# Performance work log

Hardware: AMD Instinct MI355X
Metric: run time of the kernel (lower is better)

## Reference

```python
import jax, jax.numpy as jnp
import numpy as np

ARITY = 2
DEPTH = 9          # max_depth: full tree has levels 0..DEPTH
H = 512            # hidden_size
V = 512            # vocab_size
B = 64             # batch
S = 64             # source length


def _preorder_perm(arity, depth):
    # map pre-order position -> flat level-order index
    offs = np.cumsum([0] + [arity ** d for d in range(depth + 1)])
    perm = []
    def rec(d, pos):
        perm.append(int(offs[d] + pos))
        if d < depth:
            for c in range(arity):
                rec(d + 1, pos * arity + c)
    rec(0, 0)
    return np.asarray(perm, dtype=np.int32)

PERM = jnp.asarray(_preorder_perm(ARITY, DEPTH))


def setup_inputs() -> dict:
    key = jax.random.key(0)
    ks = jax.random.split(key, 12)
    s = 0.05
    return {
        "root_hiddens": jax.random.normal(ks[0], (B, H), jnp.float32),
        "ann_emb": jax.random.normal(ks[1], (B, H), jnp.float32),
        "encoder_outputs": jax.random.normal(ks[2], (S, B, H), jnp.float32),
        "source_mask": jnp.ones((B, S), dtype=bool),
        # GRUCell params per child: input_size = 2H (attention concat)
        "w_ih": jax.random.normal(ks[3], (ARITY, 3 * H, 2 * H), jnp.float32) * s,
        "w_hh": jax.random.normal(ks[4], (ARITY, 3 * H, H), jnp.float32) * s,
        "b_ih": jax.random.normal(ks[5], (ARITY, 3 * H), jnp.float32) * s,
        "b_hh": jax.random.normal(ks[6], (ARITY, 3 * H), jnp.float32) * s,
        # hidden2vocab: Linear(H,2H) -> Sigmoid -> Linear(2H,V)
        "W1": jax.random.normal(ks[7], (2 * H, H), jnp.float32) * s,
        "b1": jax.random.normal(ks[8], (2 * H,), jnp.float32) * s,
        "W2": jax.random.normal(ks[9], (V, 2 * H), jnp.float32) * s,
        "b2": jax.random.normal(ks[10], (V,), jnp.float32) * s,
    }


def _gru(x, h, wih, whh, bih, bhh):
    # x: [B,n,2H], h: [B,n,H]; PyTorch GRUCell semantics
    gi = jnp.einsum('bni,gi->bng', x, wih) + bih
    gh = jnp.einsum('bnh,gh->bng', h, whh) + bhh
    i_r, i_z, i_n = jnp.split(gi, 3, axis=-1)
    h_r, h_z, h_n = jnp.split(gh, 3, axis=-1)
    r = jax.nn.sigmoid(i_r + h_r)
    z = jax.nn.sigmoid(i_z + h_z)
    n = jnp.tanh(i_n + r * h_n)
    return (1.0 - z) * n + z * h


def _forward(root_hiddens, ann_emb, encoder_outputs, source_mask,
             w_ih, w_hh, b_ih, b_hh, W1, b1, W2, b2):
    b = root_hiddens.shape[0]
    enc = encoder_outputs.transpose(1, 0, 2)        # [B,S,H]
    h = root_hiddens[:, None, :]                    # [B,1,H]
    prods = []
    for d in range(DEPTH + 1):
        # hidden2vocab at every node of this level
        hid = jax.nn.sigmoid(jnp.einsum('bnh,kh->bnk', h, W1) + b1)
        prods.append(jnp.einsum('bnk,vk->bnv', hid, W2) + b2)
        if d < DEPTH:
            # dot-product attention per node over source positions
            scores = jnp.einsum('bnh,bsh->bns', h, enc)
            scores = jnp.where(source_mask[:, None, :], scores, -1e9)
            a = jax.nn.softmax(scores, axis=-1)
            weighted = jnp.einsum('bns,bsh->bnh', a, enc)
            n = h.shape[1]
            x = jnp.concatenate(
                [jnp.broadcast_to(ann_emb[:, None, :], (b, n, H)), weighted],
                axis=-1)                             # [B,n,2H]
            children = [_gru(x, h, w_ih[c], w_hh[c], b_ih[c], b_hh[c])
                        for c in range(ARITY)]
            h = jnp.stack(children, axis=2).reshape(b, n * ARITY, H)
    out = jnp.concatenate(prods, axis=1)            # [B,N,V] level-order
    out = out[:, PERM, :]                           # pre-order, as torch yields
    return out.transpose(1, 0, 2)                   # [N,B,V] like pad_sequence


def reference(root_hiddens, ann_emb, encoder_outputs, source_mask,
              w_ih, w_hh, b_ih, b_hh, W1, b1, W2, b2):
    return _forward(root_hiddens, ann_emb, encoder_outputs, source_mask,
                    w_ih, w_hh, b_ih, b_hh, W1, b1, W2, b2)
```

## Files before the change

### kernel.cpp

```cpp
#include <hip/hip_runtime.h>


#define BATCH 64
#define HDIM  512

typedef float  floatx4 __attribute__((ext_vector_type(4)));
typedef float  f32x16  __attribute__((ext_vector_type(16)));
typedef short  short8  __attribute__((ext_vector_type(8)));

__device__ __forceinline__ float bf2f(unsigned short u) {
  union { unsigned int i; float f; } v; v.i = ((unsigned int)u) << 16; return v.f;
}
__device__ __forceinline__ unsigned short f2bf(float f) {
  union { float f; unsigned int i; } v; v.f = f;
  unsigned int x = v.i;
  return (unsigned short)((x + 0x7fffu + ((x >> 16) & 1u)) >> 16);
}
__device__ __forceinline__ float sigm(float x) { return 1.f / (1.f + __expf(-x)); }

__device__ __forceinline__ int preorder_idx(int d, int node) {
  int p = 0;
  for (int i = 1; i <= d; ++i) {
    int bit = (node >> (d - i)) & 1;
    p += 1 + bit * ((1 << (10 - i)) - 1);
  }
  return p;
}

__device__ __forceinline__ void gload_lds16(const void* g, void* l) {
  __builtin_amdgcn_global_load_lds(
      (const __attribute__((address_space(1))) unsigned int*)g,
      (__attribute__((address_space(3))) unsigned int*)l, 16, 0, 0);
}

__device__ __forceinline__ void stage_f32(unsigned short* ldst, const float* src) {
  float4 v0 = *(const float4*)src;
  float4 v1 = *(const float4*)(src + 4);
  union { unsigned short s[8]; float4 v; } u;
  u.s[0]=f2bf(v0.x); u.s[1]=f2bf(v0.y); u.s[2]=f2bf(v0.z); u.s[3]=f2bf(v0.w);
  u.s[4]=f2bf(v1.x); u.s[5]=f2bf(v1.y); u.s[6]=f2bf(v1.z); u.s[7]=f2bf(v1.w);
  *(float4*)ldst = u.v;
}

__device__ __forceinline__ void stage_split(unsigned short* dh, unsigned short* dl,
                                            const float* src) {
  float4 v0 = *(const float4*)src;
  float4 v1 = *(const float4*)(src + 4);
  float v[8] = {v0.x, v0.y, v0.z, v0.w, v1.x, v1.y, v1.z, v1.w};
  union { unsigned short s[8]; float4 q; } H, L;
  #pragma unroll
  for (int i = 0; i < 8; ++i) {
    unsigned short hb = f2bf(v[i]);
    H.s[i] = hb;
    L.s[i] = f2bf(v[i] - bf2f(hb));
  }
  *(float4*)dh = H.q;
  *(float4*)dl = L.q;
}

__global__ __launch_bounds__(256) void k_root(const float* __restrict__ root,
                                              float* __restrict__ h0,
                                              unsigned short* __restrict__ bh,
                                              unsigned short* __restrict__ bl) {
  int i = blockIdx.x * 256 + threadIdx.x;
  float v = root[i];
  h0[i] = v;
  int row = i >> 9, k = i & 511;
  int mt = row >> 5, r = row & 31, ktg = k >> 4, oct = (k >> 3) & 1, e = k & 7;
  size_t fo = ((size_t)(mt * 32 + ktg) * 64 + oct * 32 + r) * 8 + e;
  unsigned short hb = f2bf(v);
  bh[fo] = hb;
  bl[fo] = f2bf(v - bf2f(hb));
}

__global__ __launch_bounds__(256) void k_prep_wih(const float* __restrict__ wih,
                                                  unsigned short* __restrict__ dh,
                                                  unsigned short* __restrict__ dl) {
  int idx = blockIdx.x * 256 + threadIdx.x;
  int jr  = idx & 31;
  int oct = (idx >> 5) & 1;
  int ktg = (idx >> 6) & 31;
  int jt  = (idx >> 11) & 15;
  int cg  = idx >> 15;
  int c = cg / 3, g = cg % 3;
  int j = jt * 32 + jr, k = ktg * 16 + oct * 8;
  const float* src = wih + ((size_t)c * 1536 + g * 512 + j) * 1024 + 512 + k;
  float v[8];
  *(float4*)&v[0] = *(const float4*)src;
  *(float4*)&v[4] = *(const float4*)(src + 4);
  union { unsigned short s[8]; float4 q; } H, L;
  #pragma unroll
  for (int i = 0; i < 8; ++i) {
    unsigned short hb = f2bf(v[i]); H.s[i] = hb; L.s[i] = f2bf(v[i] - bf2f(hb));
  }
  *(float4*)(dh + (size_t)idx * 8) = H.q;
  *(float4*)(dl + (size_t)idx * 8) = L.q;
}

__global__ __launch_bounds__(256) void k_prep_whh(const float* __restrict__ whh,
                                                  unsigned short* __restrict__ dh,
                                                  unsigned short* __restrict__ dl) {
  int idx = blockIdx.x * 256 + threadIdx.x;
  int jr  = idx & 31;
  int oct = (idx >> 5) & 1;
  int ktg = (idx >> 6) & 31;
  int jt  = (idx >> 11) & 15;
  int cg  = idx >> 15;
  int c = cg / 3, g = cg % 3;
  int j = jt * 32 + jr, k = ktg * 16 + oct * 8;
  const float* src = whh + ((size_t)c * 1536 + g * 512 + j) * 512 + k;
  float v[8];
  *(float4*)&v[0] = *(const float4*)src;
  *(float4*)&v[4] = *(const float4*)(src + 4);
  union { unsigned short s[8]; float4 q; } H, L;
  #pragma unroll
  for (int i = 0; i < 8; ++i) {
    unsigned short hb = f2bf(v[i]); H.s[i] = hb; L.s[i] = f2bf(v[i] - bf2f(hb));
  }
  *(float4*)(dh + (size_t)idx * 8) = H.q;
  *(float4*)(dl + (size_t)idx * 8) = L.q;
}

__global__ __launch_bounds__(256) void k_prep_bf(const float* __restrict__ src,
                                                 unsigned short* __restrict__ db) {
  size_t i = ((size_t)blockIdx.x * 256 + threadIdx.x) * 8;
  stage_f32(db + i, src + i);
}

__global__ __launch_bounds__(256) void k_giann(const float* __restrict__ ann,
                                               const float* __restrict__ wih,
                                               float* __restrict__ giann) {
  __shared__ __align__(16) unsigned short lah[64*40], lal[64*40];
  __shared__ __align__(16) unsigned short lwh[64*40], lwl[64*40];
  int t = threadIdx.x, lane = t & 63, wv = t >> 6;
  int jbase = blockIdx.y * 64, c = blockIdx.z;
  const float* wih_c = wih + (size_t)c * 1536 * 1024;
  floatx4 acc[4];
  #pragma unroll
  for (int i = 0; i < 4; ++i) acc[i] = (floatx4)(0.f);
  int srow = t >> 2, skk = (t & 3) * 8;
  for (int k0 = 0; k0 < 512; k0 += 32) {
    stage_split(lah + srow*40 + skk, lal + srow*40 + skk,
                ann + (size_t)srow * 512 + k0 + skk);
    stage_split(lwh + srow*40 + skk, lwl + srow*40 + skk,
                wih_c + (size_t)(jbase + srow) * 1024 + k0 + skk);
    __syncthreads();
    int arow = wv * 16 + (lane & 15), kq = (lane >> 4) * 8;
    short8 ah = *(const short8*)(lah + arow*40 + kq);
    short8 al = *(const short8*)(lal + arow*40 + kq);
    #pragma unroll
    for (int nt = 0; nt < 4; ++nt) {
      int wo = (nt * 16 + (lane & 15)) * 40 + kq;
      short8 wh = *(const short8*)(lwh + wo);
      short8 wl = *(const short8*)(lwl + wo);
      acc[nt] = __builtin_amdgcn_mfma_f32_16x16x32_bf16(ah, wh, acc[nt], 0, 0, 0);
      acc[nt] = __builtin_amdgcn_mfma_f32_16x16x32_bf16(ah, wl, acc[nt], 0, 0, 0);
      acc[nt] = __builtin_amdgcn_mfma_f32_16x16x32_bf16(al, wh, acc[nt], 0, 0, 0);
    }
    __syncthreads();
  }
  int quad = lane >> 4, cl = lane & 15;
  #pragma unroll
  for (int nt = 0; nt < 4; ++nt) {
    int g = jbase + nt * 16 + cl;
    #pragma unroll
    for (int r = 0; r < 4; ++r) {
      int b = wv * 16 + quad * 4 + r;
      giann[((size_t)c * 64 + b) * 1536 + g] = acc[nt][r];
    }
  }
}

__global__ __launch_bounds__(256) void k_attn(const float* __restrict__ h,
                                              const float* __restrict__ enc,
                                              unsigned short* __restrict__ wgh,
                                              unsigned short* __restrict__ wgl,
                                              int d) {
  int lane = threadIdx.x & 63, wv = threadIdx.x >> 6;
  int m = blockIdx.x * 4 + wv;
  int b = m >> d;
  __shared__ __align__(16) float sh[4][512];
  {
    const float4* src = (const float4*)(h + (size_t)m * HDIM);
    float4* dst = (float4*)sh[wv];
    dst[lane] = src[lane];
    dst[lane + 64] = src[lane + 64];
  }
  __syncthreads();
  const float* hr = sh[wv];
  const float* er = enc + ((size_t)lane * BATCH + b) * HDIM;
  float sc = 0.f;
  for (int k = 0; k < HDIM; k += 8) {
    float4 w0 = *(const float4*)(er + k);
    float4 w1 = *(const float4*)(er + k + 4);
    sc += hr[k+0]*w0.x + hr[k+1]*w0.y + hr[k+2]*w0.z + hr[k+3]*w0.w;
    sc += hr[k+4]*w1.x + hr[k+5]*w1.y + hr[k+6]*w1.z + hr[k+7]*w1.w;
  }
  float mx = sc;
  #pragma unroll
  for (int off = 32; off; off >>= 1) mx = fmaxf(mx, __shfl_xor(mx, off));
  float e = __expf(sc - mx);
  float sum = e;
  #pragma unroll
  for (int off = 32; off; off >>= 1) sum += __shfl_xor(sum, off);
  float a = e / sum;
  float acc[8];
  #pragma unroll
  for (int i = 0; i < 8; ++i) acc[i] = 0.f;
  for (int s = 0; s < 64; ++s) {
    float as = __shfl(a, s);
    const float* ep = enc + ((size_t)s * BATCH + b) * HDIM + lane * 8;
    float4 w0 = *(const float4*)ep;
    float4 w1 = *(const float4*)(ep + 4);
    acc[0] += as * w0.x; acc[1] += as * w0.y; acc[2] += as * w0.z; acc[3] += as * w0.w;
    acc[4] += as * w1.x; acc[5] += as * w1.y; acc[6] += as * w1.z; acc[7] += as * w1.w;
  }
  union { unsigned short s[8]; float4 q; } H, L;
  #pragma unroll
  for (int i = 0; i < 8; ++i) {
    unsigned short hb = f2bf(acc[i]); H.s[i] = hb; L.s[i] = f2bf(acc[i] - bf2f(hb));
  }
  int mt = m >> 5, rr = m & 31;
  size_t fo = ((size_t)(mt * 32 + (lane >> 1)) * 64 + (lane & 1) * 32 + rr) * 8;
  *(float4*)(wgh + fo) = H.q;
  *(float4*)(wgl + fo) = L.q;
}

__global__ __launch_bounds__(256) void k_hid(const float* __restrict__ h,
                                             const unsigned short* __restrict__ W1b,
                                             const float* __restrict__ b1,
                                             unsigned short* __restrict__ hid) {
  __shared__ __align__(16) unsigned short la[64 * 40];
  __shared__ __align__(16) unsigned short lw[64 * 40];
  int t = threadIdx.x, lane = t & 63, wv = t >> 6;
  int mbase = blockIdx.x * 64, jbase = blockIdx.y * 64;
  floatx4 acc[4];
  #pragma unroll
  for (int i = 0; i < 4; ++i) acc[i] = (floatx4)(0.f);
  int srow = t >> 2, skk = (t & 3) * 8;
  for (int k0 = 0; k0 < 512; k0 += 32) {
    stage_f32(la + srow * 40 + skk, h + (size_t)(mbase + srow) * 512 + k0 + skk);
    *(float4*)(lw + srow * 40 + skk) =
        *(const float4*)(W1b + (size_t)(jbase + srow) * 512 + k0 + skk);
    __syncthreads();
    int arow = wv * 16 + (lane & 15);
    int kq = (lane >> 4) * 8;
    short8 af = *(const short8*)(la + arow * 40 + kq);
    #pragma unroll
    for (int nt = 0; nt < 4; ++nt) {
      short8 wf = *(const short8*)(lw + (nt * 16 + (lane & 15)) * 40 + kq);
      acc[nt] = __builtin_amdgcn_mfma_f32_16x16x32_bf16(af, wf, acc[nt], 0, 0, 0);
    }
    __syncthreads();
  }
  int quad = lane >> 4, cl = lane & 15;
  #pragma unroll
  for (int nt = 0; nt < 4; ++nt) {
    int j = jbase + nt * 16 + cl;
    float bias = b1[j];
    #pragma unroll
    for (int r = 0; r < 4; ++r) {
      int m = mbase + wv * 16 + quad * 4 + r;
      hid[(size_t)m * 1024 + j] = f2bf(sigm(acc[nt][r] + bias));
    }
  }
}

__global__ __launch_bounds__(256) void k_out(const unsigned short* __restrict__ hid,
                                             const unsigned short* __restrict__ W2b,
                                             const float* __restrict__ b2,
                                             float* __restrict__ out, int d) {
  __shared__ __align__(16) unsigned short la[64 * 40];
  __shared__ __align__(16) unsigned short lw[64 * 40];
  int t = threadIdx.x, lane = t & 63, wv = t >> 6;
  int mbase = blockIdx.x * 64, jbase = blockIdx.y * 64;
  floatx4 acc[4];
  #pragma unroll
  for (int i = 0; i < 4; ++i) acc[i] = (floatx4)(0.f);
  int srow = t >> 2, skk = (t & 3) * 8;
  for (int k0 = 0; k0 < 1024; k0 += 32) {
    *(float4*)(la + srow * 40 + skk) =
        *(const float4*)(hid + (size_t)(mbase + srow) * 1024 + k0 + skk);
    *(float4*)(lw + srow * 40 + skk) =
        *(const float4*)(W2b + (size_t)(jbase + srow) * 1024 + k0 + skk);
    __syncthreads();
    int arow = wv * 16 + (lane & 15);
    int kq = (lane >> 4) * 8;
    short8 af = *(const short8*)(la + arow * 40 + kq);
    #pragma unroll
    for (int nt = 0; nt < 4; ++nt) {
      short8 wf = *(const short8*)(lw + (nt * 16 + (lane & 15)) * 40 + kq);
      acc[nt] = __builtin_amdgcn_mfma_f32_16x16x32_bf16(af, wf, acc[nt], 0, 0, 0);
    }
    __syncthreads();
  }
  int quad = lane >> 4, cl = lane & 15;
  int nmask = (1 << d) - 1;
  int pv[4], bv[4];
  #pragma unroll
  for (int r = 0; r < 4; ++r) {
    int m = mbase + wv * 16 + quad * 4 + r;
    bv[r] = m >> d;
    pv[r] = preorder_idx(d, m & nmask);
  }
  #pragma unroll
  for (int nt = 0; nt < 4; ++nt) {
    int j = jbase + nt * 16 + cl;
    float bias = b2[j];
    #pragma unroll
    for (int r = 0; r < 4; ++r) {
      out[((size_t)pv[r] * BATCH + bv[r]) * 512 + j] = acc[nt][r] + bias;
    }
  }
}

#define MF32(a, b, c) __builtin_amdgcn_mfma_f32_32x32x16_bf16(a, b, c, 0, 0, 0)

__global__ __launch_bounds__(256, 2) void k_gru(const float* __restrict__ h,
                                             const unsigned short* __restrict__ wgh,
                                             const unsigned short* __restrict__ wgl,
                                             const unsigned short* __restrict__ hbh,
                                             const unsigned short* __restrict__ hbl,
                                             const unsigned short* __restrict__ wihh,
                                             const unsigned short* __restrict__ wihl,
                                             const unsigned short* __restrict__ whhh,
                                             const unsigned short* __restrict__ whhl,
                                             const float* __restrict__ bih,
                                             const float* __restrict__ bhh,
                                             const float* __restrict__ giann,
                                             float* __restrict__ hnext,
                                             unsigned short* __restrict__ nbh,
                                             unsigned short* __restrict__ nbl,
                                             int d, int M, int emit_bf) {
  __shared__ __align__(16) unsigned short smem[3][20 * 512];
  int t = threadIdx.x, lane = t & 63, wv = t >> 6;
  int wm = wv >> 1, wj = wv & 1;
  int c = blockIdx.z;
  int mbase = blockIdx.x * 128, jbase = blockIdx.y * 64;
  int jt0 = jbase >> 5;
  int mb32 = mbase >> 5;
  int mtcap = (M >> 5) - 1;

  f32x16 a_r[2], a_z[2], a_n[2], a_h[2];
  #pragma unroll
  for (int i = 0; i < 2; ++i) {
    a_r[i] = (f32x16)(0.f); a_z[i] = (f32x16)(0.f);
    a_n[i] = (f32x16)(0.f); a_h[i] = (f32x16)(0.f);
  }

  auto stage = [&](int it2, int buf2) {
    int pht = it2 >> 5, kt = it2 & 31;
    const unsigned short* Ah = pht ? hbh : wgh;
    const unsigned short* Al = pht ? hbl : wgl;
    const unsigned short* Wh = pht ? whhh : wihh;
    const unsigned short* Wl = pht ? whhl : wihl;
    #pragma unroll
    for (int q = 0; q < 5; ++q) {
      int f = wv * 5 + q;
      const unsigned short* src;
      if (f < 8) {
        int mtl = f >> 1;
        int mt = mb32 + mtl; if (mt > mtcap) mt = mtcap;
        const unsigned short* blob = (f & 1) ? Al : Ah;
        src = blob + ((size_t)(mt * 32 + kt) * 64 + lane) * 8;
      } else {
        int u = f - 8;
        int g = u >> 2, jtl = (u >> 1) & 1;
        const unsigned short* blob = (u & 1) ? Wl : Wh;
        src = blob + ((size_t)(((c * 3 + g) * 16 + jt0 + jtl) * 32 + kt) * 64
                      + lane) * 8;
      }
      gload_lds16(src, &smem[buf2][f * 512]);
    }
  };

  stage(0, 0);
  stage(1, 1);
  stage(2, 2);
  asm volatile("s_waitcnt vmcnt(10)" ::: "memory");
  __builtin_amdgcn_s_barrier();
  __builtin_amdgcn_sched_barrier(0);

  int buf = 0;
  #pragma unroll
  for (int ph = 0; ph < 2; ++ph) {
    f32x16* axr = ph ? a_h : a_n;
    for (int i2 = 0; i2 < 32; ++i2) {
      int it = ph * 32 + i2;
      const unsigned short* bb = smem[buf];
      short8 ah[2], al[2];
      #pragma unroll
      for (int mt = 0; mt < 2; ++mt) {
        int s = (wm * 2 + mt) * 2;
        ah[mt] = *(const short8*)(bb + s * 512 + lane * 8);
        al[mt] = *(const short8*)(bb + (s + 1) * 512 + lane * 8);
      }
      short8 w[3][2];
      #pragma unroll
      for (int g = 0; g < 3; ++g) {
        int s = 8 + (g * 2 + wj) * 2;
        w[g][0] = *(const short8*)(bb + s * 512 + lane * 8);
        w[g][1] = *(const short8*)(bb + (s + 1) * 512 + lane * 8);
      }
      asm volatile("s_waitcnt lgkmcnt(0)" ::: "memory");
      __builtin_amdgcn_sched_barrier(0);
      __builtin_amdgcn_s_barrier();
      __builtin_amdgcn_sched_barrier(0);
      if (it + 3 < 64) stage(it + 3, buf);
      __builtin_amdgcn_s_setprio(1);
      #pragma unroll
      for (int mt = 0; mt < 2; ++mt) {
        short8 AH = ah[mt], AL = al[mt];
        a_r[mt] = MF32(AH, w[0][0], a_r[mt]);
        a_r[mt] = MF32(AH, w[0][1], a_r[mt]);
        a_r[mt] = MF32(AL, w[0][0], a_r[mt]);
        a_z[mt] = MF32(AH, w[1][0], a_z[mt]);
        a_z[mt] = MF32(AH, w[1][1], a_z[mt]);
        a_z[mt] = MF32(AL, w[1][0], a_z[mt]);
        axr[mt] = MF32(AH, w[2][0], axr[mt]);
        axr[mt] = MF32(AH, w[2][1], axr[mt]);
        axr[mt] = MF32(AL, w[2][0], axr[mt]);
      }
      __builtin_amdgcn_s_setprio(0);
      __builtin_amdgcn_sched_barrier(0);
      if (it < 61) {
        asm volatile("s_waitcnt vmcnt(10)" ::: "memory");
      } else if (it == 61) {
        asm volatile("s_waitcnt vmcnt(5)" ::: "memory");
      } else {
        asm volatile("s_waitcnt vmcnt(0)" ::: "memory");
      }
      __builtin_amdgcn_sched_barrier(0);
      __builtin_amdgcn_s_barrier();
      __builtin_amdgcn_sched_barrier(0);
      buf = (buf == 2) ? 0 : buf + 1;
    }
  }

  unsigned short (*trh)[72] = (unsigned short(*)[72])(&smem[0][0]);
  unsigned short (*trl)[72] = (unsigned short(*)[72])(&smem[0][0] + 128 * 72);
  int cl = lane & 31;
  int j = jbase + wj * 32 + cl;
  float br  = bih[c * 1536 + j]        + bhh[c * 1536 + j];
  float bz  = bih[c * 1536 + 512 + j]  + bhh[c * 1536 + 512 + j];
  float bin = bih[c * 1536 + 1024 + j];
  float bhn = bhh[c * 1536 + 1024 + j];
  int rowoff = 4 * (lane >> 5);
  #pragma unroll
  for (int mt = 0; mt < 2; ++mt) {
    int mb0 = mbase + wm * 64 + mt * 32 + rowoff;
    #pragma unroll
    for (int r = 0; r < 16; ++r) {
      int m = mb0 + (r & 3) + 8 * (r >> 2);
      if (m < M) {
        int b = m >> d;
        const float* gp = giann + ((size_t)c * 64 + b) * 1536 + j;
        float rg = sigm(a_r[mt][r] + gp[0] + br);
        float zg = sigm(a_z[mt][r] + gp[512] + bz);
        float ng = tanhf(a_n[mt][r] + gp[1024] + bin + rg * (a_h[mt][r] + bhn));
        float hv = h[(size_t)m * 512 + j];
        float nh = (1.f - zg) * ng + zg * hv;
        hnext[(size_t)(2 * m + c) * 512 + j] = nh;
        if (emit_bf) {
          unsigned short hb = f2bf(nh);
          trh[m - mbase][j - jbase] = hb;
          trl[m - mbase][j - jbase] = f2bf(nh - bf2f(hb));
        }
      }
    }
  }
  if (emit_bf) {
    __syncthreads();
    int a = t >> 7;
    int row = t & 127;
    if (mbase + row < M) {
      const unsigned short* trp = a ? &trl[row][0] : &trh[row][0];
      unsigned short* dst = a ? nbl : nbh;
      int mp = 2 * (mbase + row) + c;
      int mtp = mp >> 5, rp = mp & 31;
      #pragma unroll
      for (int q = 0; q < 8; ++q) {
        int k = jbase + q * 8;
        int ktg = k >> 4, oct = (k >> 3) & 1;
        float4 v = *(const float4*)(trp + q * 8);
        *(float4*)(dst + ((size_t)(mtp * 32 + ktg) * 64 + oct * 32 + rp) * 8) = v;
      }
    }
  }
}

extern "C" void kernel_launch(void* const* d_in, const int* in_sizes, int n_in,
                              void* d_out, int out_size, void* d_ws, size_t ws_size,
                              hipStream_t stream) {
  const float* root = (const float*)d_in[0];
  const float* ann  = (const float*)d_in[1];
  const float* enc  = (const float*)d_in[2];
  const float* wih  = (const float*)d_in[4];
  const float* whh  = (const float*)d_in[5];
  const float* bih  = (const float*)d_in[6];
  const float* bhh  = (const float*)d_in[7];
  const float* W1   = (const float*)d_in[8];
  const float* b1   = (const float*)d_in[9];
  const float* W2   = (const float*)d_in[10];
  const float* b2   = (const float*)d_in[11];
  float* out = (float*)d_out;

  char* ws = (char*)d_ws;
  float* hA = (float*)ws;
  float* hB = (float*)(ws + (size_t)67108864);
  unsigned short* hid  = (unsigned short*)(ws + (size_t)100663296);
  unsigned short* wgh  = (unsigned short*)(ws + (size_t)134217728);
  unsigned short* wgl  = (unsigned short*)(ws + (size_t)150994944);
  unsigned short* hbEh = (unsigned short*)(ws + (size_t)167772160);
  unsigned short* hbEl = (unsigned short*)(ws + (size_t)184549376);
  unsigned short* hbOh = (unsigned short*)(ws + (size_t)201326592);
  unsigned short* hbOl = (unsigned short*)(ws + (size_t)209715200);
  float* giann         = (float*)(ws + (size_t)218103808);
  unsigned short* wihh = (unsigned short*)(ws + (size_t)218890240);
  unsigned short* wihl = (unsigned short*)(ws + (size_t)222035968);
  unsigned short* whhh = (unsigned short*)(ws + (size_t)225181696);
  unsigned short* whhl = (unsigned short*)(ws + (size_t)228327424);
  unsigned short* W1b  = (unsigned short*)(ws + (size_t)231473152);
  unsigned short* W2b  = (unsigned short*)(ws + (size_t)232521728);

  k_root<<<dim3(128), dim3(256), 0, stream>>>(root, hB, hbEh, hbEl);
  k_prep_wih<<<dim3(768), dim3(256), 0, stream>>>(wih, wihh, wihl);
  k_prep_whh<<<dim3(768), dim3(256), 0, stream>>>(whh, whhh, whhl);
  k_prep_bf<<<dim3(256), dim3(256), 0, stream>>>(W1, W1b);
  k_prep_bf<<<dim3(256), dim3(256), 0, stream>>>(W2, W2b);
  k_giann<<<dim3(1, 24, 2), dim3(256), 0, stream>>>(ann, wih, giann);

  float* hcur = hB;
  float* hnxt = hA;
  unsigned short *bhc = hbEh, *blc = hbEl, *bhn = hbOh, *bln = hbOl;
  for (int d = 0; d <= 9; ++d) {
    int n = 1 << d;
    int M = 64 * n;
    k_hid<<<dim3(M / 64, 16), dim3(256), 0, stream>>>(hcur, W1b, b1, hid);
    k_out<<<dim3(M / 64, 8), dim3(256), 0, stream>>>(hid, W2b, b2, out, d);
    if (d < 9) {
      k_attn<<<dim3(M / 4), dim3(256), 0, stream>>>(hcur, enc, wgh, wgl, d);
      k_gru<<<dim3((M + 127) / 128, 8, 2), dim3(256), 0, stream>>>(
          hcur, wgh, wgl, bhc, blc, wihh, wihl, whhh, whhl, bih, bhh, giann,
          hnxt, bhn, bln, d, M, d < 8 ? 1 : 0);
      float* tmp = hcur; hcur = hnxt; hnxt = tmp;
      unsigned short* ts;
      ts = bhc; bhc = bhn; bhn = ts;
      ts = blc; blc = bln; bln = ts;
    }
  }
}
```

Before: 2.334 ms.

## Use split-bf16 MFMA attention for deep levels and widen hid/out GEMM tiles

Adds a matrix-core attention kernel for tree depths 6 and up. Scores and the weighted sum are computed with split-bf16 (hi/lo) 32x32 MFMAs against encoder copies that are pre-transposed once per call, replacing the scalar per-node attention loop. It also widens the k_hid and k_out tiles to 256 output columns per block so each staged activation tile is reused four times. The new attention path only runs if the workspace is large enough, needs extra prep kernels and workspace, and the wider GEMM tiles produce fewer blocks at shallow levels.

Measured after the change: 1.999 ms. 14.3% less time.

```diff
diff --git a/kernel.cpp b/kernel.cpp
--- a/kernel.cpp
+++ b/kernel.cpp
@@ -121,6 +121,52 @@
   *(float4*)(dl + (size_t)idx * 8) = L.q;
 }
 
+__global__ __launch_bounds__(256) void k_prep_encB(const float* __restrict__ enc,
+                                                   unsigned short* __restrict__ dh,
+                                                   unsigned short* __restrict__ dl) {
+  int idx = blockIdx.x * 256 + threadIdx.x;
+  int jr  = idx & 31;
+  int oct = (idx >> 5) & 1;
+  int ktg = (idx >> 6) & 31;
+  int jt  = (idx >> 11) & 1;
+  int b   = idx >> 12;
+  int s = jt * 32 + jr, k = ktg * 16 + oct * 8;
+  const float* src = enc + ((size_t)s * 64 + b) * 512 + k;
+  float v[8];
+  *(float4*)&v[0] = *(const float4*)src;
+  *(float4*)&v[4] = *(const float4*)(src + 4);
+  union { unsigned short s_[8]; float4 q; } H, L;
+  #pragma unroll
+  for (int i = 0; i < 8; ++i) {
+    unsigned short hb = f2bf(v[i]); H.s_[i] = hb; L.s_[i] = f2bf(v[i] - bf2f(hb));
+  }
+  *(float4*)(dh + (size_t)idx * 8) = H.q;
+  *(float4*)(dl + (size_t)idx * 8) = L.q;
+}
+
+__global__ __launch_bounds__(256) void k_prep_encT(const float* __restrict__ enc,
+                                                   unsigned short* __restrict__ dh,
+                                                   unsigned short* __restrict__ dl) {
+  int idx = blockIdx.x * 256 + threadIdx.x;
+  int jr  = idx & 31;
+  int oct = (idx >> 5) & 1;
+  int ktg = (idx >> 6) & 3;
+  int jt  = (idx >> 8) & 15;
+  int b   = idx >> 12;
+  int hcol = jt * 32 + jr, s0 = ktg * 16 + oct * 8;
+  float v[8];
+  #pragma unroll
+  for (int e = 0; e < 8; ++e)
+    v[e] = enc[((size_t)(s0 + e) * 64 + b) * 512 + hcol];
+  union { unsigned short s_[8]; float4 q; } H, L;
+  #pragma unroll
+  for (int i = 0; i < 8; ++i) {
+    unsigned short hb = f2bf(v[i]); H.s_[i] = hb; L.s_[i] = f2bf(v[i] - bf2f(hb));
+  }
+  *(float4*)(dh + (size_t)idx * 8) = H.q;
+  *(float4*)(dl + (size_t)idx * 8) = L.q;
+}
+
 __global__ __launch_bounds__(256) void k_prep_bf(const float* __restrict__ src,
                                                  unsigned short* __restrict__ db) {
   size_t i = ((size_t)blockIdx.x * 256 + threadIdx.x) * 8;
@@ -226,44 +272,185 @@
   *(float4*)(wgl + fo) = L.q;
 }
 
+#define MF32(a, b, c) __builtin_amdgcn_mfma_f32_32x32x16_bf16(a, b, c, 0, 0, 0)
+
+__global__ __launch_bounds__(256, 1) void k_attn_mfma(
+    const unsigned short* __restrict__ hbh, const unsigned short* __restrict__ hbl,
+    const unsigned short* __restrict__ encBh, const unsigned short* __restrict__ encBl,
+    const unsigned short* __restrict__ encTh, const unsigned short* __restrict__ encTl,
+    unsigned short* __restrict__ wgh, unsigned short* __restrict__ wgl, int d) {
+  __shared__ __align__(16) float Sf[4608];
+  __shared__ __align__(16) unsigned short PAh[4096], PAl[4096];
+  int t = threadIdx.x, lane = t & 63, wv = t >> 6;
+  int mbase = blockIdx.x * 64;
+  int b = mbase >> d;
+  int mtg0 = mbase >> 5;
+  {
+    int mt = wv >> 1, sh2 = wv & 1;
+    f32x16 acc = (f32x16)(0.f);
+    size_t ab = ((size_t)(mtg0 + mt) * 32) * 512;
+    size_t bb = ((size_t)(b * 2 + sh2) * 32) * 512;
+    #pragma unroll 4
+    for (int kt = 0; kt < 32; ++kt) {
+      size_t o = ((size_t)kt * 64 + lane) * 8;
+      short8 ah = *(const short8*)(hbh + ab + o);
+      short8 al = *(const short8*)(hbl + ab + o);
+      short8 bh = *(const short8*)(encBh + bb + o);
+      short8 bl = *(const short8*)(encBl + bb + o);
+      acc = MF32(ah, bh, acc);
+      acc = MF32(ah, bl, acc);
+      acc = MF32(al, bh, acc);
+    }
+    int col = sh2 * 32 + (lane & 31);
+    int rb = mt * 32 + 4 * (lane >> 5);
+    #pragma unroll
+    for (int r = 0; r < 16; ++r)
+      Sf[(rb + (r & 3) + 8 * (r >> 2)) * 68 + col] = acc[r];
+  }
+  __syncthreads();
+  {
+    int row = t >> 2, q = t & 3;
+    float v[16];
+    const float* Sr = Sf + row * 68 + q * 16;
+    *(float4*)&v[0]  = *(const float4*)(Sr);
+    *(float4*)&v[4]  = *(const float4*)(Sr + 4);
+    *(float4*)&v[8]  = *(const float4*)(Sr + 8);
+    *(float4*)&v[12] = *(const float4*)(Sr + 12);
+    float mx = v[0];
+    #pragma unroll
+    for (int i = 1; i < 16; ++i) mx = fmaxf(mx, v[i]);
+    mx = fmaxf(mx, __shfl_xor(mx, 1));
+    mx = fmaxf(mx, __shfl_xor(mx, 2));
+    float sum = 0.f;
+    #pragma unroll
+    for (int i = 0; i < 16; ++i) { v[i] = __expf(v[i] - mx); sum += v[i]; }
+    sum += __shfl_xor(sum, 1);
+    sum += __shfl_xor(sum, 2);
+    float inv = 1.f / sum;
+    int wbase = ((row >> 5) * 4 + q) * 64;
+    #pragma unroll
+    for (int oct = 0; oct < 2; ++oct) {
+      union { unsigned short s_[8]; float4 q4; } H, L;
+      #pragma unroll
+      for (int e = 0; e < 8; ++e) {
+        float a = v[oct * 8 + e] * inv;
+        unsigned short hb = f2bf(a);
+        H.s_[e] = hb; L.s_[e] = f2bf(a - bf2f(hb));
+      }
+      int w = (wbase + oct * 32 + (row & 31)) * 8;
+      *(float4*)(PAh + w) = H.q4;
+      *(float4*)(PAl + w) = L.q4;
+    }
+  }
+  __syncthreads();
+  f32x16 o2[2][4];
+  #pragma unroll
+  for (int mt = 0; mt < 2; ++mt)
+    #pragma unroll
+    for (int jl = 0; jl < 4; ++jl) o2[mt][jl] = (f32x16)(0.f);
+  #pragma unroll
+  for (int ktg = 0; ktg < 4; ++ktg) {
+    short8 pah[2], pal[2];
+    #pragma unroll
+    for (int mt = 0; mt < 2; ++mt) {
+      pah[mt] = *(const short8*)(PAh + ((mt * 4 + ktg) * 64 + lane) * 8);
+      pal[mt] = *(const short8*)(PAl + ((mt * 4 + ktg) * 64 + lane) * 8);
+    }
+    #pragma unroll
+    for (int jl = 0; jl < 4; ++jl) {
+      int jt = wv * 4 + jl;
+      size_t eb = (((size_t)(b * 16 + jt) * 4 + ktg) * 64 + lane) * 8;
+      short8 ebh = *(const short8*)(encTh + eb);
+      short8 ebl = *(const short8*)(encTl + eb);
+      #pragma unroll
+      for (int mt = 0; mt < 2; ++mt) {
+        o2[mt][jl] = MF32(pah[mt], ebh, o2[mt][jl]);
+        o2[mt][jl] = MF32(pah[mt], ebl, o2[mt][jl]);
+        o2[mt][jl] = MF32(pal[mt], ebh, o2[mt][jl]);
+      }
+    }
+  }
+  float* scr = Sf + wv * 1152;
+  int jrr = lane & 31, oct = lane >> 5;
+  #pragma unroll
+  for (int mt = 0; mt < 2; ++mt) {
+    #pragma unroll
+    for (int jl = 0; jl < 4; ++jl) {
+      int col = lane & 31;
+      int rb = 4 * (lane >> 5);
+      #pragma unroll
+      for (int r = 0; r < 16; ++r)
+        scr[(rb + (r & 3) + 8 * (r >> 2)) * 36 + col] = o2[mt][jl][r];
+      asm volatile("s_waitcnt lgkmcnt(0)" ::: "memory");
+      __builtin_amdgcn_sched_barrier(0);
+      int jt = wv * 4 + jl;
+      #pragma unroll
+      for (int kh = 0; kh < 2; ++kh) {
+        float vv[8];
+        const float* sp = scr + jrr * 36 + kh * 16 + oct * 8;
+        *(float4*)&vv[0] = *(const float4*)sp;
+        *(float4*)&vv[4] = *(const float4*)(sp + 4);
+        union { unsigned short s_[8]; float4 q4; } H, L;
+        #pragma unroll
+        for (int e = 0; e < 8; ++e) {
+          unsigned short hb = f2bf(vv[e]);
+          H.s_[e] = hb; L.s_[e] = f2bf(vv[e] - bf2f(hb));
+        }
+        size_t wo = (((size_t)(mtg0 + mt) * 32 + (jt * 2 + kh)) * 64 + lane) * 8;
+        *(float4*)(wgh + wo) = H.q4;
+        *(float4*)(wgl + wo) = L.q4;
+      }
+      asm volatile("s_waitcnt lgkmcnt(0)" ::: "memory");
+    }
+  }
+}
+
 __global__ __launch_bounds__(256) void k_hid(const float* __restrict__ h,
                                              const unsigned short* __restrict__ W1b,
                                              const float* __restrict__ b1,
                                              unsigned short* __restrict__ hid) {
   __shared__ __align__(16) unsigned short la[64 * 40];
-  __shared__ __align__(16) unsigned short lw[64 * 40];
+  __shared__ __align__(16) unsigned short lw[4][64 * 40];
   int t = threadIdx.x, lane = t & 63, wv = t >> 6;
-  int mbase = blockIdx.x * 64, jbase = blockIdx.y * 64;
-  floatx4 acc[4];
-  #pragma unroll
-  for (int i = 0; i < 4; ++i) acc[i] = (floatx4)(0.f);
+  int mbase = blockIdx.x * 64, jbase = blockIdx.y * 256;
+  floatx4 acc[4][4];
+  #pragma unroll
+  for (int jt = 0; jt < 4; ++jt)
+    #pragma unroll
+    for (int i = 0; i < 4; ++i) acc[jt][i] = (floatx4)(0.f);
   int srow = t >> 2, skk = (t & 3) * 8;
   for (int k0 = 0; k0 < 512; k0 += 32) {
     stage_f32(la + srow * 40 + skk, h + (size_t)(mbase + srow) * 512 + k0 + skk);
-    *(float4*)(lw + srow * 40 + skk) =
-        *(const float4*)(W1b + (size_t)(jbase + srow) * 512 + k0 + skk);
+    #pragma unroll
+    for (int jt = 0; jt < 4; ++jt)
+      *(float4*)(lw[jt] + srow * 40 + skk) =
+          *(const float4*)(W1b + (size_t)(jbase + jt * 64 + srow) * 512 + k0 + skk);
     __syncthreads();
     int arow = wv * 16 + (lane & 15);
     int kq = (lane >> 4) * 8;
     short8 af = *(const short8*)(la + arow * 40 + kq);
     #pragma unroll
+    for (int jt = 0; jt < 4; ++jt)
+      #pragma unroll
+      for (int nt = 0; nt < 4; ++nt) {
+        short8 wf = *(const short8*)(lw[jt] + (nt * 16 + (lane & 15)) * 40 + kq);
+        acc[jt][nt] = __builtin_amdgcn_mfma_f32_16x16x32_bf16(af, wf, acc[jt][nt], 0, 0, 0);
+      }
+    __syncthreads();
+  }
+  int quad = lane >> 4, cl = lane & 15;
+  #pragma unroll
+  for (int jt = 0; jt < 4; ++jt)
+    #pragma unroll
     for (int nt = 0; nt < 4; ++nt) {
-      short8 wf = *(const short8*)(lw + (nt * 16 + (lane & 15)) * 40 + kq);
-      acc[nt] = __builtin_amdgcn_mfma_f32_16x16x32_bf16(af, wf, acc[nt], 0, 0, 0);
-    }
-    __syncthreads();
-  }
-  int quad = lane >> 4, cl = lane & 15;
-  #pragma unroll
-  for (int nt = 0; nt < 4; ++nt) {
-    int j = jbase + nt * 16 + cl;
-    float bias = b1[j];
-    #pragma unroll
-    for (int r = 0; r < 4; ++r) {
-      int m = mbase + wv * 16 + quad * 4 + r;
-      hid[(size_t)m * 1024 + j] = f2bf(sigm(acc[nt][r] + bias));
-    }
-  }
+      int j = jbase + jt * 64 + nt * 16 + cl;
+      float bias = b1[j];
+      #pragma unroll
+      for (int r = 0; r < 4; ++r) {
+        int m = mbase + wv * 16 + quad * 4 + r;
+        hid[(size_t)m * 1024 + j] = f2bf(sigm(acc[jt][nt][r] + bias));
+      }
+    }
 }
 
 __global__ __launch_bounds__(256) void k_out(const unsigned short* __restrict__ hid,
@@ -271,27 +458,33 @@
                                              const float* __restrict__ b2,
                                              float* __restrict__ out, int d) {
   __shared__ __align__(16) unsigned short la[64 * 40];
-  __shared__ __align__(16) unsigned short lw[64 * 40];
+  __shared__ __align__(16) unsigned short lw[4][64 * 40];
   int t = threadIdx.x, lane = t & 63, wv = t >> 6;
-  int mbase = blockIdx.x * 64, jbase = blockIdx.y * 64;
-  floatx4 acc[4];
-  #pragma unroll
-  for (int i = 0; i < 4; ++i) acc[i] = (floatx4)(0.f);
+  int mbase = blockIdx.x * 64, jbase = blockIdx.y * 256;
+  floatx4 acc[4][4];
+  #pragma unroll
+  for (int jt = 0; jt < 4; ++jt)
+    #pragma unroll
+    for (int i = 0; i < 4; ++i) acc[jt][i] = (floatx4)(0.f);
   int srow = t >> 2, skk = (t & 3) * 8;
   for (int k0 = 0; k0 < 1024; k0 += 32) {
     *(float4*)(la + srow * 40 + skk) =
         *(const float4*)(hid + (size_t)(mbase + srow) * 1024 + k0 + skk);
-    *(float4*)(lw + srow * 40 + skk) =
-        *(const float4*)(W2b + (size_t)(jbase + srow) * 1024 + k0 + skk);
+    #pragma unroll
+    for (int jt = 0; jt < 4; ++jt)
+      *(float4*)(lw[jt] + srow * 40 + skk) =
+          *(const float4*)(W2b + (size_t)(jbase + jt * 64 + srow) * 1024 + k0 + skk);
     __syncthreads();
     int arow = wv * 16 + (lane & 15);
     int kq = (lane >> 4) * 8;
     short8 af = *(const short8*)(la + arow * 40 + kq);
     #pragma unroll
-    for (int nt = 0; nt < 4; ++nt) {
-      short8 wf = *(const short8*)(lw + (nt * 16 + (lane & 15)) * 40 + kq);
-      acc[nt] = __builtin_amdgcn_mfma_f32_16x16x32_bf16(af, wf, acc[nt], 0, 0, 0);
-    }
+    for (int jt = 0; jt < 4; ++jt)
+      #pragma unroll
+      for (int nt = 0; nt < 4; ++nt) {
+        short8 wf = *(const short8*)(lw[jt] + (nt * 16 + (lane & 15)) * 40 + kq);
+        acc[jt][nt] = __builtin_amdgcn_mfma_f32_16x16x32_bf16(af, wf, acc[jt][nt], 0, 0, 0);
+      }
     __syncthreads();
   }
   int quad = lane >> 4, cl = lane & 15;
@@ -304,17 +497,17 @@
     pv[r] = preorder_idx(d, m & nmask);
   }
   #pragma unroll
-  for (int nt = 0; nt < 4; ++nt) {
-    int j = jbase + nt * 16 + cl;
-    float bias = b2[j];
-    #pragma unroll
-    for (int r = 0; r < 4; ++r) {
-      out[((size_t)pv[r] * BATCH + bv[r]) * 512 + j] = acc[nt][r] + bias;
-    }
-  }
-}
-
-#define MF32(a, b, c) __builtin_amdgcn_mfma_f32_32x32x16_bf16(a, b, c, 0, 0, 0)
+  for (int jt = 0; jt < 4; ++jt)
+    #pragma unroll
+    for (int nt = 0; nt < 4; ++nt) {
+      int j = jbase + jt * 64 + nt * 16 + cl;
+      float bias = b2[j];
+      #pragma unroll
+      for (int r = 0; r < 4; ++r) {
+        out[((size_t)pv[r] * BATCH + bv[r]) * 512 + j] = acc[jt][nt][r] + bias;
+      }
+    }
+}
 
 __global__ __launch_bounds__(256, 2) void k_gru(const float* __restrict__ h,
                                              const unsigned short* __restrict__ wgh,
@@ -522,12 +715,21 @@
   unsigned short* whhl = (unsigned short*)(ws + (size_t)228327424);
   unsigned short* W1b  = (unsigned short*)(ws + (size_t)231473152);
   unsigned short* W2b  = (unsigned short*)(ws + (size_t)232521728);
+  unsigned short* encBh = (unsigned short*)(ws + (size_t)234881024);
+  unsigned short* encBl = (unsigned short*)(ws + (size_t)239075328);
+  unsigned short* encTh = (unsigned short*)(ws + (size_t)243269632);
+  unsigned short* encTl = (unsigned short*)(ws + (size_t)247463936);
+  int use_mfma_attn = (ws_size >= (size_t)251658240) ? 1 : 0;
 
   k_root<<<dim3(128), dim3(256), 0, stream>>>(root, hB, hbEh, hbEl);
   k_prep_wih<<<dim3(768), dim3(256), 0, stream>>>(wih, wihh, wihl);
   k_prep_whh<<<dim3(768), dim3(256), 0, stream>>>(whh, whhh, whhl);
   k_prep_bf<<<dim3(256), dim3(256), 0, stream>>>(W1, W1b);
   k_prep_bf<<<dim3(256), dim3(256), 0, stream>>>(W2, W2b);
+  if (use_mfma_attn) {
+    k_prep_encB<<<dim3(1024), dim3(256), 0, stream>>>(enc, encBh, encBl);
+    k_prep_encT<<<dim3(1024), dim3(256), 0, stream>>>(enc, encTh, encTl);
+  }
   k_giann<<<dim3(1, 24, 2), dim3(256), 0, stream>>>(ann, wih, giann);
 
   float* hcur = hB;
@@ -536,10 +738,15 @@
   for (int d = 0; d <= 9; ++d) {
     int n = 1 << d;
     int M = 64 * n;
-    k_hid<<<dim3(M / 64, 16), dim3(256), 0, stream>>>(hcur, W1b, b1, hid);
-    k_out<<<dim3(M / 64, 8), dim3(256), 0, stream>>>(hid, W2b, b2, out, d);
+    k_hid<<<dim3(M / 64, 4), dim3(256), 0, stream>>>(hcur, W1b, b1, hid);
+    k_out<<<dim3(M / 64, 2), dim3(256), 0, stream>>>(hid, W2b, b2, out, d);
     if (d < 9) {
-      k_attn<<<dim3(M / 4), dim3(256), 0, stream>>>(hcur, enc, wgh, wgl, d);
+      if (use_mfma_attn && d >= 6) {
+        k_attn_mfma<<<dim3(M / 64), dim3(256), 0, stream>>>(
+            bhc, blc, encBh, encBl, encTh, encTl, wgh, wgl, d);
+      } else {
+        k_attn<<<dim3(M / 4), dim3(256), 0, stream>>>(hcur, enc, wgh, wgl, d);
+      }
       k_gru<<<dim3((M + 127) / 128, 8, 2), dim3(256), 0, stream>>>(
           hcur, wgh, wgl, bhc, blc, wihh, wihl, whhh, whhl, bih, bhh, giann,
           hnxt, bhn, bln, d, M, d < 8 ? 1 : 0);
```
